# Kernel optimization log

Hardware: AMD Instinct MI355X
Metric: run time of the kernel (lower is better)

## Reference

```python
import jax, jax.numpy as jnp
import numpy as np
from jax import lax

T, B = 64, 16
N, W, R = 256, 64, 4          # mem_slot, mem_size, read_heads
IN, OUT = 64, 64
NHID, NNOUT = 256, 256
IF_SIZE = W * R + 3 * W + 5 * R + 3  # 471
EPS = 1e-6


def setup_inputs() -> dict:
    key = jax.random.key(0)
    ks = jax.random.split(key, 8)
    in_dim = IN + R * W
    def glorot(k, shape):
        fan_in = shape[0]
        return jax.random.normal(k, shape, dtype=jnp.float32) / np.sqrt(fan_in)
    return {
        "input_data": jax.random.normal(ks[0], (T, B, IN), dtype=jnp.float32),
        "W1": glorot(ks[1], (in_dim, NHID)),
        "b1": jnp.zeros((NHID,), jnp.float32),
        "W2": glorot(ks[2], (NHID, NNOUT)),
        "b2": jnp.zeros((NNOUT,), jnp.float32),
        "W_if": glorot(ks[3], (NNOUT, IF_SIZE)),
        "b_if": jnp.zeros((IF_SIZE,), jnp.float32),
        "W_out": glorot(ks[4], (NNOUT, OUT)),
        "W_mem_out": glorot(ks[5], (R * W, OUT)),
    }


def oneplus(x):
    return 1.0 + jax.nn.softplus(x)


def content_address(mem, keys, strengths):
    # mem [B,N,W], keys [B,W,R], strengths [B,R] -> weights [B,N,R]
    mem_n = mem / (jnp.linalg.norm(mem, axis=-1, keepdims=True) + EPS)
    key_n = keys / (jnp.linalg.norm(keys, axis=1, keepdims=True) + EPS)
    sim = jnp.einsum('bnw,bwr->bnr', mem_n, key_n)
    return jax.nn.softmax(sim * strengths[:, None, :], axis=1)


def parse_interface(z):
    # z: [B, IF_SIZE] -> dict of interface components (NeuCom layout)
    o = 0
    read_keys = z[:, o:o + W * R].reshape(-1, W, R); o += W * R
    read_str = oneplus(z[:, o:o + R]); o += R
    write_key = z[:, o:o + W]; o += W
    write_str = oneplus(z[:, o:o + 1]); o += 1
    erase = jax.nn.sigmoid(z[:, o:o + W]); o += W
    write_vec = z[:, o:o + W]; o += W
    free_gates = jax.nn.sigmoid(z[:, o:o + R]); o += R
    alloc_gate = jax.nn.sigmoid(z[:, o:o + 1]); o += 1
    write_gate = jax.nn.sigmoid(z[:, o:o + 1]); o += 1
    read_modes = jax.nn.softmax(z[:, o:o + 3 * R].reshape(-1, 3, R), axis=1)
    return (read_keys, read_str, write_key, write_str, erase, write_vec,
            free_gates, alloc_gate, write_gate, read_modes)


def _dnc_forward(input_data, W1, b1, W2, b2, W_if, b_if, W_out, W_mem_out):
    Bz = input_data.shape[1]
    eye = jnp.eye(N, dtype=input_data.dtype)

    def step(carry, x_t):
        mem, usage, rw, ww, prec, link, rvec = carry
        # --- controller (feedforward) ---
        ctrl_in = jnp.concatenate([x_t, rvec.reshape(Bz, R * W)], axis=1)
        h = jnp.tanh(ctrl_in @ W1 + b1)
        nn_out = jnp.tanh(h @ W2 + b2)
        (read_keys, read_str, write_key, write_str, erase, write_vec,
         free_gates, alloc_gate, write_gate, read_modes) = parse_interface(nn_out @ W_if + b_if)
        # --- write ---
        retention = jnp.prod(1.0 - free_gates[:, None, :] * rw, axis=2)   # [B,N]
        usage = (usage + ww - usage * ww) * retention
        idx = jnp.argsort(usage, axis=1)                                  # ascending usage
        u_sorted = jnp.take_along_axis(usage, idx, axis=1)
        prod_excl = jnp.concatenate(
            [jnp.ones((Bz, 1), usage.dtype), jnp.cumprod(u_sorted, axis=1)[:, :-1]], axis=1)
        alloc_sorted = (1.0 - u_sorted) * prod_excl
        alloc = jnp.take_along_axis(alloc_sorted, jnp.argsort(idx, axis=1), axis=1)
        wc = content_address(mem, write_key[:, :, None], write_str)[:, :, 0]  # [B,N]
        ww = write_gate * (alloc_gate * alloc + (1.0 - alloc_gate) * wc)
        mem = mem * (1.0 - ww[:, :, None] * erase[:, None, :]) \
              + ww[:, :, None] * write_vec[:, None, :]
        link = (1.0 - ww[:, :, None] - ww[:, None, :]) * link \
               + ww[:, :, None] * prec[:, None, :]
        link = link * (1.0 - eye)
        prec = (1.0 - jnp.sum(ww, axis=1, keepdims=True)) * prec + ww
        # --- read ---
        rc = content_address(mem, read_keys, read_str)                    # [B,N,R]
        fwd_w = jnp.einsum('bnm,bmr->bnr', link, rw)
        bwd_w = jnp.einsum('bmn,bmr->bnr', link, rw)
        rw = (bwd_w * read_modes[:, 0][:, None, :]
              + rc * read_modes[:, 1][:, None, :]
              + fwd_w * read_modes[:, 2][:, None, :])
        rvec = jnp.einsum('bnw,bnr->bwr', mem, rw)                        # [B,W,R]
        out = nn_out @ W_out + rvec.reshape(Bz, R * W) @ W_mem_out
        view = (free_gates, alloc_gate, write_gate, rw, ww, usage)
        return (mem, usage, rw, ww, prec, link, rvec), (out, view)

    carry0 = (
        jnp.full((Bz, N, W), EPS, input_data.dtype),   # mem_mat
        jnp.zeros((Bz, N), input_data.dtype),          # usage
        jnp.zeros((Bz, N, R), input_data.dtype),       # read_weight
        jnp.zeros((Bz, N), input_data.dtype),          # write_weight
        jnp.zeros((Bz, N), input_data.dtype),          # precedence
        jnp.zeros((Bz, N, N), input_data.dtype),       # link matrix
        jnp.zeros((Bz, W, R), input_data.dtype),       # read vectors
    )
    _, (outputs, _view) = lax.scan(step, carry0, input_data)
    return outputs  # [T,B,OUT]


def reference(input_data, W1, b1, W2, b2, W_if, b_if, W_out, W_mem_out):
    return _dnc_forward(input_data, W1, b1, W2, b2, W_if, b_if, W_out, W_mem_out)
```

## Files before the change

### kernel.cpp

```cpp
#include <hip/hip_runtime.h>
#include <hip/hip_fp16.h>
#include <math.h>

#define Tt 64
#define Bb 16
#define Nn 256
#define Ww 64
#define Rr 4
#define INd 64
#define OUTd 64
#define IFS 471
#define EPSf 1e-6f

#define W1OFF   0
#define W2OFF   40960
#define WIFOFF  73728
#define WOUTOFF 134016
#define WMEMOFF 142208
#define WTOT    150400

#define LROW    129
#define LINKB   (256 * LROW * 4)
#define SCRB    16384
#define FIXF    3456
#define SMEM_MAIN (LINKB + SCRB + FIXF * 4)
#define SMEM_FB   (SCRB + FIXF * 4)

#define RWS 132

typedef _Float16 h2v __attribute__((ext_vector_type(2)));
__device__ __forceinline__ float fdot2(__half2 a, __half2 b, float c) {
    return __builtin_amdgcn_fdot2(*(h2v*)&a, *(h2v*)&b, c, false);
}
__device__ __forceinline__ __half2 pkh(float a, float b) {
    auto r = __builtin_amdgcn_cvt_pkrtz(a, b);
    return *(__half2*)&r;
}

__device__ __forceinline__ float sigm(float x) { return 1.f / (1.f + expf(-x)); }
__device__ __forceinline__ float oneplus_(float x) {
    return 1.f + fmaxf(x, 0.f) + log1pf(expf(-fabsf(x)));
}
__device__ __forceinline__ float wsum(float v) {
#pragma unroll
    for (int o = 32; o; o >>= 1) v += __shfl_xor(v, o, 64);
    return v;
}
__device__ __forceinline__ float wmaxr(float v) {
#pragma unroll
    for (int o = 32; o; o >>= 1) v = fmaxf(v, __shfl_xor(v, o, 64));
    return v;
}

__device__ __attribute__((noinline)) float gemv_part(
    const __half2* __restrict__ wP, int str, int iters,
    const __half2* __restrict__ vin)
{
    float a[8] = {0.f,0.f,0.f,0.f,0.f,0.f,0.f,0.f};
#pragma unroll 1
    for (int j0 = 0; j0 < iters; j0 += 8) {
        __half2 hh[8], vv[8];
        int k8 = j0 >> 2;
        *(float4*)&hh[0] = *(const float4*)(wP + (size_t)k8 * str);
        *(float4*)&hh[4] = *(const float4*)(wP + (size_t)(k8 + 1) * str);
        *(float4*)&vv[0] = *(const float4*)(vin + j0);
        *(float4*)&vv[4] = *(const float4*)(vin + j0 + 4);
#pragma unroll
        for (int u = 0; u < 8; ++u) a[u] = fdot2(hh[u], vv[u], a[u]);
    }
    return ((a[0]+a[1])+(a[2]+a[3])) + ((a[4]+a[5])+(a[6]+a[7]));
}

__global__ void convert_weights(const float* __restrict__ W1, const float* __restrict__ W2,
                                const float* __restrict__ Wif, const float* __restrict__ Wout,
                                const float* __restrict__ Wmem, __half2* __restrict__ wp) {
    int i = blockIdx.x * blockDim.x + threadIdx.x;
    if (i >= WTOT) return;
    float a, b;
    if (i < W2OFF) {
        int q = i & 3, s = i >> 2, n = s & 255, k2 = (s >> 8) * 4 + q;
        a = W1[(2*k2)*256+n];  b = W1[(2*k2+1)*256+n];
    } else if (i < WIFOFF) {
        int t = i - W2OFF;
        int q = t & 3, s = t >> 2, n = s & 255, k2 = (s >> 8) * 4 + q;
        a = W2[(2*k2)*256+n];  b = W2[(2*k2+1)*256+n];
    } else if (i < WOUTOFF) {
        int t = i - WIFOFF;
        int q = t & 3, s = t >> 2, o = s % IFS, k2 = (s / IFS) * 4 + q;
        a = Wif[(2*k2)*IFS+o]; b = Wif[(2*k2+1)*IFS+o];
    } else if (i < WMEMOFF) {
        int t = i - WOUTOFF;
        int q = t & 3, s = t >> 2, n = s & 63, k2 = (s >> 6) * 4 + q;
        a = Wout[(2*k2)*64+n]; b = Wout[(2*k2+1)*64+n];
    } else {
        int t = i - WMEMOFF;
        int q = t & 3, s = t >> 2, n = s & 63, k2 = (s >> 6) * 4 + q;
        a = Wmem[(2*k2)*64+n]; b = Wmem[(2*k2+1)*64+n];
    }
    wp[i] = __floats2half2_rn(a, b);
}

template <bool LLINK>
__global__ __launch_bounds__(1024) void dnc_kernel(
    const float* __restrict__ x, const float* __restrict__ b1,
    const float* __restrict__ b2, const float* __restrict__ bif,
    const __half2* __restrict__ wp,
    __half* __restrict__ memg,
    __half2* __restrict__ memWg,
    __half2* __restrict__ linkg,
    float* __restrict__ out)
{
    extern __shared__ __align__(16) char smem[];
    const int b = blockIdx.x;
    const int tid = threadIdx.x;
    const int lane = tid & 63;
    const int wv = tid >> 6;

    __half2* l2p = (__half2*)smem;
    __half2* gl2 = linkg + (size_t)b * (256 * LROW);
    float* scr   = (float*)(smem + (LLINK ? LINKB : 0));
    __half* scrh = (__half*)scr;
    float* fx    = (float*)((char*)scr + SCRB);

    float*   s_rw    = fx + 0;
    __half2* s_ctrlh = (__half2*)(fx + 1024);
    __half2* s_hh    = (__half2*)(fx + 1184);
    __half2* s_nnh   = (__half2*)(fx + 1312);
    __half2* s_rwh   = (__half2*)(fx + 1440);
    float* s_z     = fx + 1968;
    float* s_usage = fx + 2440;
    float* s_ww    = fx + 2696;
    float* s_prec  = fx + 2952;
    float* s_knorm = fx + 3208;
    float* s_rstr  = fx + 3212;
    float* s_rmode = fx + 3216;
    float* s_sc    = fx + 3228;
    float* s_red   = fx + 3232;
    float* s_er    = fx + 3264;
    __half2* s_keyh = (__half2*)(fx + 3328);
    float* s_srt   = scr + 1024;
    float* s_cp    = scr + 1280;
    __half2* s_keyw2 = (__half2*)(scr + 1280);
    float* s_wcdot = scr + 1536;
    float* s_wcss  = scr + 1792;

    __half*  memh  = memg + (size_t)b * (Ww * Nn);
    __half2* memh2 = (__half2*)memh;
    __half2* memW2 = memWg + (size_t)b * (32 * 256);
    __half*  memWh = (__half*)memW2;

    auto lread = [&](int idx) -> __half2 {
        if constexpr (LLINK) return l2p[idx]; else return gl2[idx];
    };
    auto lwrite = [&](int idx, __half2 v) {
        if constexpr (LLINK) l2p[idx] = v; else gl2[idx] = v;
    };

    {
        __half2 z2 = pkh(0.f, 0.f);
#pragma unroll 1
        for (int i = tid; i < 256 * LROW; i += 1024) lwrite(i, z2);
        __half2 e2 = __floats2half2_rn(EPSf, EPSf);
#pragma unroll 1
        for (int j = 0; j < 8; ++j) { memh2[tid + j * 1024] = e2; memW2[tid + j * 1024] = e2; }
        if (tid < 528) s_rwh[tid] = z2;
        if (tid < 32) {
            float2 xv = *(const float2*)&x[b * INd + 2 * tid];
            s_ctrlh[tid] = pkh(xv.x, xv.y);
        } else if (tid < 160) s_ctrlh[tid] = z2;
    }
    if (tid < 256) {
        s_usage[tid] = 0.f; s_ww[tid] = 0.f; s_prec[tid] = 0.f;
        s_rw[tid*4+0] = 0.f; s_rw[tid*4+1] = 0.f; s_rw[tid*4+2] = 0.f; s_rw[tid*4+3] = 0.f;
    }

#pragma unroll 1
    for (int t = 0; t < Tt; ++t) {
        __syncthreads();

        {
            int kc = wv >> 2, o = (wv & 3) * 64 + lane;
            scr[kc * 256 + o] = gemv_part(wp + W1OFF + o * 4 + kc * 10240, 1024, 40,
                                          s_ctrlh + kc * 40);
        }
        __syncthreads();
        if (tid < 256) {
            float v = tanhf(b1[tid] + ((scr[tid] + scr[256+tid]) + (scr[512+tid] + scr[768+tid])));
            float pv = __shfl_xor(v, 1, 64);
            if ((tid & 1) == 0) s_hh[tid >> 1] = pkh(v, pv);
        }
        __syncthreads();

        {
            int kc = wv >> 2, o = (wv & 3) * 64 + lane;
            scr[kc * 256 + o] = gemv_part(wp + W2OFF + o * 4 + kc * 8192, 1024, 32,
                                          s_hh + kc * 32);
        }
        __syncthreads();
        if (tid < 256) {
            float v = tanhf(b2[tid] + ((scr[tid] + scr[256+tid]) + (scr[512+tid] + scr[768+tid])));
            float pv = __shfl_xor(v, 1, 64);
            if ((tid & 1) == 0) s_nnh[tid >> 1] = pkh(v, pv);
        }
        __syncthreads();

        {
            int kc = wv >> 3, o = (wv & 7) * 64 + lane;
            if (o < IFS)
                scr[kc * 512 + o] = gemv_part(wp + WIFOFF + o * 4 + kc * 30144, 1884, 64,
                                              s_nnh + kc * 64);
        }
        __syncthreads();
        if (tid < IFS) {
            float v = bif[tid] + scr[tid] + scr[512 + tid];
            s_z[tid] = v;
            float pv1 = __shfl_xor(v, 1, 64);
            float pv4 = __shfl_xor(v, 4, 64);
            if (tid < 256) {
                if ((tid & 4) == 0)
                    s_keyh[(tid & 3) * 32 + (tid >> 3)] = pkh(v, pv4);
            } else if (tid >= 260 && tid < 324) {
                if ((tid & 1) == 0)
                    s_keyw2[(tid - 260) >> 1] = pkh(v, pv1);
            }
        }
        __syncthreads();

        if (wv < 4) {
            float vz = s_z[lane * 4 + wv];
            float s = wsum(vz * vz);
            if (lane == 0) s_knorm[wv] = sqrtf(s) + EPSf;
        } else if (wv == 4) {
            float vz = s_z[260 + lane];
            float s = wsum(vz * vz);
            if (lane == 0) s_sc[3] = sqrtf(s) + EPSf;
        } else if (wv == 5) {
            if (lane < 4) s_rstr[lane] = oneplus_(s_z[256 + lane]);
            else if (lane >= 8 && lane < 12) {
                int r = lane - 8;
                float a = s_z[459+r], bm = s_z[463+r], c = s_z[467+r];
                float mx = fmaxf(a, fmaxf(bm, c));
                float ea = expf(a-mx), eb = expf(bm-mx), ec = expf(c-mx);
                float inv = 1.f / ((ea+eb)+ec);
                s_rmode[0*4+r] = ea*inv; s_rmode[1*4+r] = eb*inv; s_rmode[2*4+r] = ec*inv;
            } else if (lane == 16) s_sc[0] = oneplus_(s_z[324]);
            else if (lane == 17) s_sc[1] = sigm(s_z[457]);
            else if (lane == 18) s_sc[2] = sigm(s_z[458]);
        } else if (wv == 6) {
            s_er[lane] = sigm(s_z[325 + lane]);
        } else if (wv >= 8 && wv < 12) {
            int n = tid - 512;
            float ret = 1.f;
#pragma unroll
            for (int r = 0; r < 4; ++r) {
                float fg = sigm(s_z[453 + r]);
                ret *= 1.f - fg * s_rw[n*4 + r];
            }
            float u = s_usage[n], wwo = s_ww[n];
            s_usage[n] = (u + wwo - u * wwo) * ret;
        } else if (wv >= 12) {
            int n = tid - 768;
            const __half2* mW = memW2 + n;
            float dot = 0.f, ssv = 0.f;
#pragma unroll 1
            for (int c = 0; c < 32; c += 8) {
                __half2 mv[8], kv[8];
#pragma unroll
                for (int u = 0; u < 8; ++u) mv[u] = mW[(c + u) * 256];
                *(float4*)&kv[0] = *(const float4*)(s_keyw2 + c);
                *(float4*)&kv[4] = *(const float4*)(s_keyw2 + c + 4);
#pragma unroll
                for (int u = 0; u < 8; ++u) {
                    ssv = fdot2(mv[u], mv[u], ssv);
                    dot = fdot2(mv[u], kv[u], dot);
                }
            }
            s_wcdot[n] = dot; s_wcss[n] = ssv;
        }
        __syncthreads();

        {
            int q = tid >> 8, n = tid & 255;
            float un = s_usage[n];
            float cnt = 0.f;
            int j0 = q * 64;
#pragma unroll 1
            for (int j = j0; j < j0 + 64; j += 4) {
                float4 uv = *(const float4*)&s_usage[j];
                cnt += (uv.x < un || (uv.x == un && j     < n)) ? 1.f : 0.f;
                cnt += (uv.y < un || (uv.y == un && j + 1 < n)) ? 1.f : 0.f;
                cnt += (uv.z < un || (uv.z == un && j + 2 < n)) ? 1.f : 0.f;
                cnt += (uv.w < un || (uv.w == un && j + 3 < n)) ? 1.f : 0.f;
            }
            scr[q * 256 + n] = cnt;
        }
        __syncthreads();

        if (wv == 0) {
            int rk[4]; float uu[4];
#pragma unroll
            for (int i = 0; i < 4; ++i) {
                int n = lane * 4 + i;
                float c = scr[n] + scr[256+n] + scr[512+n] + scr[768+n];
                rk[i] = (int)(c + 0.5f);
                uu[i] = s_usage[n];
                s_srt[rk[i]] = uu[i];
            }
            float4 vs = ((const float4*)s_srt)[lane];
            float p1 = vs.x * vs.y, p2 = p1 * vs.z, tot = p2 * vs.w;
            float incl = tot;
#pragma unroll
            for (int off = 1; off < 64; off <<= 1) {
                float tv = __shfl_up(incl, off, 64);
                if (lane >= off) incl *= tv;
            }
            float excl = __shfl_up(incl, 1, 64);
            if (lane == 0) excl = 1.f;
            float4 o4v; o4v.x = excl; o4v.y = excl*vs.x; o4v.z = excl*p1; o4v.w = excl*p2;
            ((float4*)s_cp)[lane] = o4v;

            float sims[4], mx = -1e30f;
#pragma unroll
            for (int i = 0; i < 4; ++i) {
                int n = lane * 4 + i;
                sims[i] = s_wcdot[n] / ((sqrtf(s_wcss[n]) + EPSf) * s_sc[3]) * s_sc[0];
                mx = fmaxf(mx, sims[i]);
            }
            mx = wmaxr(mx);
            float es[4], ls = 0.f;
#pragma unroll
            for (int i = 0; i < 4; ++i) { es[i] = expf(sims[i] - mx); ls += es[i]; }
            ls = wsum(ls);
            float ag = s_sc[1], wg = s_sc[2], inv = 1.f / ls, lw = 0.f;
#pragma unroll
            for (int i = 0; i < 4; ++i) {
                int n = lane * 4 + i;
                float alloc = (1.f - uu[i]) * s_cp[rk[i]];
                float wwn = wg * (ag * alloc + (1.f - ag) * es[i] * inv);
                s_ww[n] = wwn; lw += wwn;
            }
            lw = wsum(lw);
            if (lane == 0) s_red[0] = lw;
        }
        __syncthreads();

        if (tid < 512) {
            int kc = tid >> 7, p = tid & 127;
            int c0 = 2 * p, c1 = c0 + 1;
            float wwc0 = s_ww[c0], wwc1 = s_ww[c1];
            float pt0 = s_prec[c0], pt1 = s_prec[c1];
            float acc[8] = {0,0,0,0,0,0,0,0};
            int kbase = kc * 64;
#pragma unroll 1
            for (int k0 = kbase; k0 < kbase + 64; k0 += 8) {
                __half2 lv[8];
#pragma unroll
                for (int u = 0; u < 8; ++u) lv[u] = lread((k0 + u) * LROW + p);
                float wk8[8];
                *(float4*)&wk8[0] = *(const float4*)&s_ww[k0];
                *(float4*)&wk8[4] = *(const float4*)&s_ww[k0 + 4];
                float l0v[8], l1v[8];
#pragma unroll
                for (int u = 0; u < 8; ++u) {
                    int k = k0 + u;
                    float wk = wk8[u];
                    float2 lf = __half22float2(lv[u]);
                    float l0 = (1.f - wk - wwc0) * lf.x + wk * pt0;
                    float l1 = (1.f - wk - wwc1) * lf.y + wk * pt1;
                    if (k == c0) l0 = 0.f;
                    if (k == c1) l1 = 0.f;
                    l0v[u] = l0; l1v[u] = l1;
                }
#pragma unroll
                for (int u = 0; u < 8; ++u)
                    lwrite((k0 + u) * LROW + p, pkh(l0v[u], l1v[u]));
                __half2 l0p[4], l1p[4];
#pragma unroll
                for (int i = 0; i < 4; ++i) {
                    l0p[i] = pkh(l0v[2*i], l0v[2*i+1]);
                    l1p[i] = pkh(l1v[2*i], l1v[2*i+1]);
                }
                int kp0 = k0 >> 1;
#pragma unroll
                for (int r = 0; r < 4; ++r) {
                    __half2 rp[4];
                    *(float4*)rp = *(const float4*)(s_rwh + r * RWS + kp0);
#pragma unroll
                    for (int i = 0; i < 4; ++i) {
                        acc[r]     = fdot2(l0p[i], rp[i], acc[r]);
                        acc[4 + r] = fdot2(l1p[i], rp[i], acc[4 + r]);
                    }
                }
            }
            __half2* bp = (__half2*)scrh + (kc * 128 + p) * 4;
            bp[0] = pkh(acc[0], acc[1]);
            bp[1] = pkh(acc[2], acc[3]);
            bp[2] = pkh(acc[4], acc[5]);
            bp[3] = pkh(acc[6], acc[7]);
        } else {
            int t0 = tid - 512;
#pragma unroll 1
            for (int jb = 0; jb < 2; ++jb) {
                __half2 mv[8];
#pragma unroll
                for (int j = 0; j < 8; ++j) mv[j] = memh2[t0 + (jb * 8 + j) * 512];
#pragma unroll
                for (int j = 0; j < 8; ++j) {
                    int i2 = t0 + (jb * 8 + j) * 512;
                    int w = i2 >> 7, n2 = i2 & 127;
                    float er = s_er[w];
                    float wvv = s_z[389 + w];
                    float2 mf = __half22float2(mv[j]);
                    float wa = s_ww[2*n2], wb = s_ww[2*n2 + 1];
                    mf.x = mf.x * (1.f - wa * er) + wa * wvv;
                    mf.y = mf.y * (1.f - wb * er) + wb * wvv;
                    __half2 hv = __floats2half2_rn(mf.x, mf.y);
                    memh2[i2] = hv;
                    int wb2 = (w >> 1) * 512 + 4 * n2 + (w & 1);
                    memWh[wb2]     = __low2half(hv);
                    memWh[wb2 + 2] = __high2half(hv);
                }
            }
        }
        __syncthreads();

        {
            int q = tid >> 8, n8 = tid & 255;
            float f[4] = {0.f, 0.f, 0.f, 0.f};
            int base = n8 * LROW + q * 32;
#pragma unroll 1
            for (int j0 = 0; j0 < 32; j0 += 8) {
                __half2 lv[8];
#pragma unroll
                for (int u = 0; u < 8; ++u) lv[u] = lread(base + j0 + u);
#pragma unroll
                for (int r = 0; r < 4; ++r) {
                    __half2 rp[8];
                    *(float4*)&rp[0] = *(const float4*)(s_rwh + r * RWS + q * 32 + j0);
                    *(float4*)&rp[4] = *(const float4*)(s_rwh + r * RWS + q * 32 + j0 + 4);
#pragma unroll
                    for (int u = 0; u < 8; ++u) f[r] = fdot2(lv[u], rp[u], f[r]);
                }
            }
            __half2* fp2 = (__half2*)(scrh + 4096) + (q * 256 + n8) * 2;
            fp2[0] = pkh(f[0], f[1]);
            fp2[1] = pkh(f[2], f[3]);
            if (q == 0) s_prec[n8] = (1.f - s_red[0]) * s_prec[n8] + s_ww[n8];
        }
        __syncthreads();

        int rr = tid >> 8, n8c = tid & 255;
        float bwv = 0.f, fwv = 0.f, e_rc = 0.f;
        {
#pragma unroll
            for (int kc = 0; kc < 4; ++kc)
                bwv += __half2float(scrh[(kc * 128 + (n8c >> 1)) * 8 + (n8c & 1) * 4 + rr]);
#pragma unroll
            for (int qq = 0; qq < 4; ++qq)
                fwv += __half2float(scrh[4096 + (qq * 256 + n8c) * 4 + rr]);
            const __half2* mW = memW2 + n8c;
            const __half2* kh = s_keyh + rr * 32;
            float ssv = 0.f, dv = 0.f;
#pragma unroll 1
            for (int c = 0; c < 32; c += 8) {
                __half2 mv[8], kv[8];
#pragma unroll
                for (int u = 0; u < 8; ++u) mv[u] = mW[(c + u) * 256];
                *(float4*)&kv[0] = *(const float4*)(kh + c);
                *(float4*)&kv[4] = *(const float4*)(kh + c + 4);
#pragma unroll
                for (int u = 0; u < 8; ++u) {
                    ssv = fdot2(mv[u], mv[u], ssv);
                    dv  = fdot2(mv[u], kv[u], dv);
                }
            }
            float sim = dv / ((sqrtf(ssv) + EPSf) * s_knorm[rr]) * s_rstr[rr];
            e_rc = expf(sim);
            float s = wsum(e_rc);
            if (lane == 0) s_red[16 + wv] = s;
        }
        __syncthreads();
        {
            float sm = (s_red[16+rr*4+0] + s_red[16+rr*4+1]) + (s_red[16+rr*4+2] + s_red[16+rr*4+3]);
            float rc = e_rc / sm;
            float v = bwv * s_rmode[0*4+rr] + rc * s_rmode[1*4+rr] + fwv * s_rmode[2*4+rr];
            s_rw[n8c*4 + rr] = v;
            float pv = __shfl_xor(v, 1, 64);
            if ((n8c & 1) == 0) s_rwh[rr * RWS + (n8c >> 1)] = pkh(v, pv);
        }
        __syncthreads();

        {
            int kc = tid >> 8, o = tid & 255, w = o >> 2, r = o & 3;
            const __half2* mw2 = (const __half2*)(memh + w * 256 + kc * 64);
            const __half2* rw2 = s_rwh + r * RWS + kc * 32;
            float a = 0.f;
#pragma unroll
            for (int c = 0; c < 8; ++c) {
                __half2 mv[4], rv[4];
                *(float4*)mv = *(const float4*)(mw2 + c * 4);
                *(float4*)rv = *(const float4*)(rw2 + c * 4);
#pragma unroll
                for (int u = 0; u < 4; ++u) a = fdot2(mv[u], rv[u], a);
            }
            scr[kc * 256 + o] = a;
        }
        __syncthreads();

        if (tid < 256) {
            float v = (scr[tid] + scr[256+tid]) + (scr[512+tid] + scr[768+tid]);
            float pv = __shfl_xor(v, 1, 64);
            if ((tid & 1) == 0) s_ctrlh[32 + (tid >> 1)] = pkh(v, pv);
        } else if (tid >= 512 && tid < 544) {
            if (t + 1 < Tt) {
                int i = tid - 512;
                float2 xv = *(const float2*)&x[((t + 1) * Bb + b) * INd + 2 * i];
                s_ctrlh[i] = pkh(xv.x, xv.y);
            }
        }
        __syncthreads();

        {
            int c4 = wv, o4 = lane;
            const __half2* wsrc = (c4 < 8) ? (wp + WOUTOFF + o4 * 4 + c4 * 1024)
                                           : (wp + WMEMOFF + o4 * 4 + (c4 - 8) * 1024);
            const __half2* vsrc = (c4 < 8) ? (s_nnh + c4 * 16)
                                           : (s_ctrlh + 32 + (c4 - 8) * 16);
            scr[c4 * 64 + o4] = gemv_part(wsrc, 256, 16, vsrc);
        }
        __syncthreads();
        if (tid < 64) {
            float s = 0.f;
#pragma unroll
            for (int g = 0; g < 16; ++g) s += scr[g * 64 + tid];
            out[(t * Bb + b) * OUTd + tid] = s;
        }
    }
}

extern "C" void kernel_launch(void* const* d_in, const int* in_sizes, int n_in,
                              void* d_out, int out_size, void* d_ws, size_t ws_size,
                              hipStream_t stream) {
    const float* x    = (const float*)d_in[0];
    const float* W1   = (const float*)d_in[1];
    const float* b1   = (const float*)d_in[2];
    const float* W2   = (const float*)d_in[3];
    const float* b2   = (const float*)d_in[4];
    const float* Wif  = (const float*)d_in[5];
    const float* bif  = (const float*)d_in[6];
    const float* Wout = (const float*)d_in[7];
    const float* Wmem = (const float*)d_in[8];
    float* out = (float*)d_out;

    char* ws = (char*)d_ws;
    __half2* wp    = (__half2*)ws;
    __half*  memg  = (__half*)(ws + 601600);
    __half2* memWg = (__half2*)(ws + 601600 + 524288);
    __half2* linkg = (__half2*)(ws + 601600 + 524288 + 524288);

    convert_weights<<<dim3((WTOT + 255) / 256), dim3(256), 0, stream>>>(W1, W2, Wif, Wout, Wmem, wp);

    hipError_t rc = hipFuncSetAttribute(
        reinterpret_cast<const void*>(&dnc_kernel<true>),
        hipFuncAttributeMaxDynamicSharedMemorySize, SMEM_MAIN);
    if (rc == hipSuccess) {
        dnc_kernel<true><<<dim3(Bb), dim3(1024), SMEM_MAIN, stream>>>(
            x, b1, b2, bif, wp, memg, memWg, linkg, out);
    } else {
        dnc_kernel<false><<<dim3(Bb), dim3(1024), SMEM_FB, stream>>>(
            x, b1, b2, bif, wp, memg, memWg, linkg, out);
    }
}
```

Measured before the change: 1.880 ms.

## Compute link update in packed half2 and software-pipeline gemv weight loads

The link-matrix update inner loop now runs in packed fp16 (hfma2/hsub2), using precomputed half2 broadcasts of write weights and (1-ww) kept in shared scratch. The per-element diagonal masking is removed from the hot loop and replaced by a fix-up pass that zeroes the diagonal entries and subtracts their contribution from the accumulators. Separately, gemv_part prefetches the next weight rows one iteration ahead to hide load latency. The half-precision arithmetic lowers the accuracy of the link values, and the diagonal correction relies on s_rw matching the packed read weights.

```diff
diff --git a/kernel.cpp b/kernel.cpp
--- a/kernel.cpp
+++ b/kernel.cpp
@@ -57,16 +57,36 @@
     const __half2* __restrict__ vin)
 {
     float a[8] = {0.f,0.f,0.f,0.f,0.f,0.f,0.f,0.f};
-#pragma unroll 1
-    for (int j0 = 0; j0 < iters; j0 += 8) {
-        __half2 hh[8], vv[8];
-        int k8 = j0 >> 2;
-        *(float4*)&hh[0] = *(const float4*)(wP + (size_t)k8 * str);
-        *(float4*)&hh[4] = *(const float4*)(wP + (size_t)(k8 + 1) * str);
-        *(float4*)&vv[0] = *(const float4*)(vin + j0);
-        *(float4*)&vv[4] = *(const float4*)(vin + j0 + 4);
-#pragma unroll
-        for (int u = 0; u < 8; ++u) a[u] = fdot2(hh[u], vv[u], a[u]);
+    float4 h0 = *(const float4*)(wP);
+    float4 h1 = *(const float4*)(wP + str);
+#pragma unroll 1
+    for (int j0 = 0; j0 < iters - 8; j0 += 8) {
+        int k8n = (j0 >> 2) + 2;
+        float4 n0 = *(const float4*)(wP + (size_t)k8n * str);
+        float4 n1 = *(const float4*)(wP + (size_t)(k8n + 1) * str);
+        float4 v0 = *(const float4*)(vin + j0);
+        float4 v1 = *(const float4*)(vin + j0 + 4);
+        const __half2* hh0 = (const __half2*)&h0;
+        const __half2* hh1 = (const __half2*)&h1;
+        const __half2* vv0 = (const __half2*)&v0;
+        const __half2* vv1 = (const __half2*)&v1;
+#pragma unroll
+        for (int u = 0; u < 4; ++u) a[u]     = fdot2(hh0[u], vv0[u], a[u]);
+#pragma unroll
+        for (int u = 0; u < 4; ++u) a[4 + u] = fdot2(hh1[u], vv1[u], a[4 + u]);
+        h0 = n0; h1 = n1;
+    }
+    {
+        float4 v0 = *(const float4*)(vin + iters - 8);
+        float4 v1 = *(const float4*)(vin + iters - 4);
+        const __half2* hh0 = (const __half2*)&h0;
+        const __half2* hh1 = (const __half2*)&h1;
+        const __half2* vv0 = (const __half2*)&v0;
+        const __half2* vv1 = (const __half2*)&v1;
+#pragma unroll
+        for (int u = 0; u < 4; ++u) a[u]     = fdot2(hh0[u], vv0[u], a[u]);
+#pragma unroll
+        for (int u = 0; u < 4; ++u) a[4 + u] = fdot2(hh1[u], vv1[u], a[4 + u]);
     }
     return ((a[0]+a[1])+(a[2]+a[3])) + ((a[4]+a[5])+(a[6]+a[7]));
 }
@@ -143,6 +163,8 @@
     __half2* s_keyw2 = (__half2*)(scr + 1280);
     float* s_wcdot = scr + 1536;
     float* s_wcss  = scr + 1792;
+    __half2* s_wwh2 = (__half2*)(scr + 2048);
+    __half2* s_tmh2 = (__half2*)(scr + 2304);
 
     __half*  memh  = memg + (size_t)b * (Ww * Nn);
     __half2* memh2 = (__half2*)memh;
@@ -338,6 +360,8 @@
                 float alloc = (1.f - uu[i]) * s_cp[rk[i]];
                 float wwn = wg * (ag * alloc + (1.f - ag) * es[i] * inv);
                 s_ww[n] = wwn; lw += wwn;
+                s_wwh2[n] = pkh(wwn, wwn);
+                s_tmh2[n] = pkh(1.f - wwn, 1.f - wwn);
             }
             lw = wsum(lw);
             if (lane == 0) s_red[0] = lw;
@@ -347,40 +371,35 @@
         if (tid < 512) {
             int kc = tid >> 7, p = tid & 127;
             int c0 = 2 * p, c1 = c0 + 1;
-            float wwc0 = s_ww[c0], wwc1 = s_ww[c1];
-            float pt0 = s_prec[c0], pt1 = s_prec[c1];
+            __half2 wwcp = pkh(s_ww[c0], s_ww[c1]);
+            __half2 ptp  = pkh(s_prec[c0], s_prec[c1]);
             float acc[8] = {0,0,0,0,0,0,0,0};
             int kbase = kc * 64;
 #pragma unroll 1
             for (int k0 = kbase; k0 < kbase + 64; k0 += 8) {
-                __half2 lv[8];
+                __half2 lv[8], tm[8], wk[8];
 #pragma unroll
                 for (int u = 0; u < 8; ++u) lv[u] = lread((k0 + u) * LROW + p);
-                float wk8[8];
-                *(float4*)&wk8[0] = *(const float4*)&s_ww[k0];
-                *(float4*)&wk8[4] = *(const float4*)&s_ww[k0 + 4];
-                float l0v[8], l1v[8];
-#pragma unroll
-                for (int u = 0; u < 8; ++u) {
-                    int k = k0 + u;
-                    float wk = wk8[u];
-                    float2 lf = __half22float2(lv[u]);
-                    float l0 = (1.f - wk - wwc0) * lf.x + wk * pt0;
-                    float l1 = (1.f - wk - wwc1) * lf.y + wk * pt1;
-                    if (k == c0) l0 = 0.f;
-                    if (k == c1) l1 = 0.f;
-                    l0v[u] = l0; l1v[u] = l1;
+                *(float4*)&tm[0] = *(const float4*)(s_tmh2 + k0);
+                *(float4*)&tm[4] = *(const float4*)(s_tmh2 + k0 + 4);
+                *(float4*)&wk[0] = *(const float4*)(s_wwh2 + k0);
+                *(float4*)&wk[4] = *(const float4*)(s_wwh2 + k0 + 4);
+                __half2 ln[8];
+#pragma unroll
+                for (int u = 0; u < 8; ++u)
+                    ln[u] = __hfma2(__hsub2(tm[u], wwcp), lv[u], __hmul2(wk[u], ptp));
+#pragma unroll
+                for (int u = 0; u < 8; ++u)
+                    lwrite((k0 + u) * LROW + p, ln[u]);
+                int kp0 = k0 >> 1;
+                __half2 l0p[4], l1p[4];
+#pragma unroll
+                for (int i = 0; i < 4; ++i) {
+                    unsigned ua = *(unsigned*)&ln[2*i], ub = *(unsigned*)&ln[2*i+1];
+                    unsigned r0 = __builtin_amdgcn_perm(ub, ua, 0x05040100u);
+                    unsigned r1 = __builtin_amdgcn_perm(ub, ua, 0x07060302u);
+                    l0p[i] = *(__half2*)&r0; l1p[i] = *(__half2*)&r1;
                 }
-#pragma unroll
-                for (int u = 0; u < 8; ++u)
-                    lwrite((k0 + u) * LROW + p, pkh(l0v[u], l1v[u]));
-                __half2 l0p[4], l1p[4];
-#pragma unroll
-                for (int i = 0; i < 4; ++i) {
-                    l0p[i] = pkh(l0v[2*i], l0v[2*i+1]);
-                    l1p[i] = pkh(l1v[2*i], l1v[2*i+1]);
-                }
-                int kp0 = k0 >> 1;
 #pragma unroll
                 for (int r = 0; r < 4; ++r) {
                     __half2 rp[4];
@@ -390,6 +409,21 @@
                         acc[r]     = fdot2(l0p[i], rp[i], acc[r]);
                         acc[4 + r] = fdot2(l1p[i], rp[i], acc[4 + r]);
                     }
+                }
+            }
+            if ((c0 >> 6) == kc) {
+                __half2 d0 = lread(c0 * LROW + p);
+                __half2 d1 = lread(c1 * LROW + p);
+                float dl0 = __half2float(__low2half(d0));
+                float dl1 = __half2float(__high2half(d1));
+                unsigned u0 = *(unsigned*)&d0; u0 &= 0xFFFF0000u;
+                unsigned u1 = *(unsigned*)&d1; u1 &= 0x0000FFFFu;
+                lwrite(c0 * LROW + p, *(__half2*)&u0);
+                lwrite(c1 * LROW + p, *(__half2*)&u1);
+#pragma unroll
+                for (int r = 0; r < 4; ++r) {
+                    acc[r]     = fmaf(-dl0, s_rw[c0*4 + r], acc[r]);
+                    acc[4 + r] = fmaf(-dl1, s_rw[c1*4 + r], acc[4 + r]);
                 }
             }
             __half2* bp = (__half2*)scrh + (kc * 128 + p) * 4;
```

Result: faster. 1.837 ms (-2.3%).
